# Performance work log

Hardware: AMD Instinct MI355X
Metric: run time of the kernel (lower is better)

The kernel has to match this reference:

```python
import jax, jax.numpy as jnp
import numpy as np

DIM = 1024
INTER = 1024
E = 8            # n_routed_experts
TOP_K = 2        # n_activated_experts
ROUTE_SCALE = 1.0
B, S = 2, 1024


def setup_inputs() -> dict:
    key = jax.random.key(0)
    ks = jax.random.split(key, 8)
    scale = 0.02
    x = jax.random.normal(ks[0], (B, S, DIM), dtype=jnp.float32)
    gate_w = jax.random.normal(ks[1], (DIM, E), dtype=jnp.float32) * scale
    w1 = jax.random.normal(ks[2], (E, DIM, INTER), dtype=jnp.float32) * scale
    w2 = jax.random.normal(ks[3], (E, INTER, DIM), dtype=jnp.float32) * scale
    w3 = jax.random.normal(ks[4], (E, DIM, INTER), dtype=jnp.float32) * scale
    sw1 = jax.random.normal(ks[5], (DIM, INTER), dtype=jnp.float32) * scale
    sw2 = jax.random.normal(ks[6], (INTER, DIM), dtype=jnp.float32) * scale
    sw3 = jax.random.normal(ks[7], (DIM, INTER), dtype=jnp.float32) * scale
    return {"x": x, "gate_w": gate_w, "w1": w1, "w2": w2, "w3": w3,
            "sw1": sw1, "sw2": sw2, "sw3": sw3}


def reference(x, gate_w, w1, w2, w3, sw1, sw2, sw3):
    b, s, d = x.shape
    xt = x.reshape(-1, d)                      # [T, D]
    T = xt.shape[0]

    # --- TokenChoiceTopKRouter (score_func='softmax') ---
    scores = jax.nn.softmax((xt @ gate_w).astype(jnp.float32), axis=-1)  # [T, E]
    top_scores, top_idx = jax.lax.top_k(scores, TOP_K)                   # [T, K]
    top_scores = top_scores * ROUTE_SCALE

    # Dense combine weights [T, E]: scatter top-k routing weights per token.
    cw = jnp.zeros((T, E), dtype=xt.dtype)
    cw = cw.at[jnp.arange(T)[:, None], top_idx].set(top_scores.astype(xt.dtype))

    # --- GroupedExperts: SwiGLU per routed expert ---
    h1 = jnp.einsum('td,edh->teh', xt, w1)     # [T, E, INTER]
    h3 = jnp.einsum('td,edh->teh', xt, w3)
    h = jax.nn.silu(h1) * h3
    expert_out = jnp.einsum('teh,ehd->ted', h, w2)   # [T, E, D]

    # Combine: weighted sum over activated experts (zero weight elsewhere).
    routed = jnp.einsum('ted,te->td', expert_out, cw)

    # --- Shared expert (runs on all tokens) ---
    shared = (jax.nn.silu(xt @ sw1) * (xt @ sw3)) @ sw2

    return (routed + shared).reshape(b, s, d)
```

## Files before the change

### kernel.cpp

```cpp
#include <hip/hip_runtime.h>
#include <hip/hip_bf16.h>
#include <cstdint>
#include <cstddef>

#define DIM   1024
#define INTER 1024
#define NT    2048

typedef __attribute__((ext_vector_type(4))) float  f32x4;
typedef __attribute__((ext_vector_type(8))) short  s16x8;
typedef __attribute__((ext_vector_type(8))) unsigned short u16x8;

#define WS_CNT    0u
#define WS_SLOT   256u
#define WS_ASSIGN 33024u
#define WS_WT     65792u
#define WS_WTS2   98560u
#define WS_XB     131584u
#define WS_H      4325888u
#define WS_W1T    16908800u
#define WS_W3T    33686016u
#define WS_W2T    50463232u
#define WS_SW1T   67240448u
#define WS_SW3T   69337600u
#define WS_SW2T   71434752u
#define WS_NEED   73531904u
#define WS_OBUF   WS_W1T

__device__ __forceinline__ unsigned short f2bf(float f) {
    unsigned int u = __float_as_uint(f);
    return (unsigned short)((u + 0x7fffu + ((u >> 16) & 1u)) >> 16);
}
__device__ __forceinline__ float bf2f(unsigned short v) {
    return __uint_as_float(((unsigned int)v) << 16);
}

__device__ __forceinline__ void cp16(const void* g, void* l) {
    __builtin_amdgcn_global_load_lds((const __attribute__((address_space(1))) void*)g,
                                     (__attribute__((address_space(3))) void*)l, 16, 0, 0);
}

__device__ __forceinline__ void conv_tile(const float* __restrict__ src,
                                          unsigned short* __restrict__ dst,
                                          int r0, int c0, char* smem)
{
    float (*tile)[64][65] = (float (*)[64][65])smem;
    int tid = threadIdx.x;
    int lr = tid >> 2, lcg = (tid & 3) * 16;
    #pragma unroll
    for (int h = 0; h < 2; ++h) {
        const f32x4* srow = (const f32x4*)(src + (size_t)(r0 + lr) * 1024 + c0 + h * 64 + lcg);
        #pragma unroll
        for (int q = 0; q < 4; ++q) {
            f32x4 v = srow[q];
            #pragma unroll
            for (int j = 0; j < 4; ++j) tile[h][lr][lcg + q * 4 + j] = v[j];
        }
    }
    __syncthreads();
    int dc = tid >> 2, dkg = (tid & 3) * 16;
    #pragma unroll
    for (int h = 0; h < 2; ++h) {
        u16x8 o0, o1;
        #pragma unroll
        for (int j = 0; j < 8; ++j) o0[j] = f2bf(tile[h][dkg + j][dc]);
        #pragma unroll
        for (int j = 0; j < 8; ++j) o1[j] = f2bf(tile[h][dkg + 8 + j][dc]);
        u16x8* drow = (u16x8*)(dst + (size_t)(c0 + h * 64 + dc) * 1024 + r0 + dkg);
        drow[0] = o0; drow[1] = o1;
    }
}

__global__ __launch_bounds__(256) void kfat1(
    const float* __restrict__ x, const float* __restrict__ gw,
    const float* __restrict__ w1, const float* __restrict__ w3,
    const float* __restrict__ sw1, const float* __restrict__ sw3,
    unsigned short* __restrict__ w1t, unsigned short* __restrict__ w3t,
    unsigned short* __restrict__ sw1t, unsigned short* __restrict__ sw3t,
    int* __restrict__ assign, float2* __restrict__ wts2, unsigned short* __restrict__ xb)
{
    __shared__ __align__(16) char smem[33280];
    int bid = blockIdx.x;
    if (bid < 2304) {
        int slab = bid >> 7, t = bid & 127;
        int r0 = (t >> 3) * 64, c0 = (t & 7) * 128;
        const float* src; unsigned short* dst;
        if (slab < 8)        { src = w1 + (size_t)slab * DIM * INTER;       dst = w1t + (size_t)slab * DIM * INTER; }
        else if (slab < 16)  { src = w3 + (size_t)(slab - 8) * DIM * INTER; dst = w3t + (size_t)(slab - 8) * DIM * INTER; }
        else if (slab == 16) { src = sw1; dst = sw1t; }
        else                 { src = sw3; dst = sw3t; }
        conv_tile(src, dst, r0, c0, smem);
        return;
    }
    int wid = threadIdx.x >> 6, lane = threadIdx.x & 63;
    int t = (bid - 2304) * 4 + wid;
    const float* xrow = x + (size_t)t * DIM;

    float xr[16];
    float acc[8] = {0.f,0.f,0.f,0.f,0.f,0.f,0.f,0.f};
    #pragma unroll
    for (int j = 0; j < 16; ++j) {
        float xv = xrow[j * 64 + lane];
        xr[j] = xv;
        const f32x4* g = (const f32x4*)(gw + (size_t)(j * 64 + lane) * 8);
        f32x4 g0 = g[0], g1 = g[1];
        acc[0] += xv * g0[0]; acc[1] += xv * g0[1]; acc[2] += xv * g0[2]; acc[3] += xv * g0[3];
        acc[4] += xv * g1[0]; acc[5] += xv * g1[1]; acc[6] += xv * g1[2]; acc[7] += xv * g1[3];
    }
    #pragma unroll
    for (int j = 0; j < 16; ++j) xb[(size_t)t * DIM + j * 64 + lane] = f2bf(xr[j]);

    #pragma unroll
    for (int e = 0; e < 8; ++e) {
        float v = acc[e];
        v += __shfl_xor(v, 1);  v += __shfl_xor(v, 2);  v += __shfl_xor(v, 4);
        v += __shfl_xor(v, 8);  v += __shfl_xor(v, 16); v += __shfl_xor(v, 32);
        acc[e] = v;
    }
    float mx = acc[0];
    #pragma unroll
    for (int e = 1; e < 8; ++e) mx = fmaxf(mx, acc[e]);
    float p[8]; float se = 0.f;
    #pragma unroll
    for (int e = 0; e < 8; ++e) { p[e] = expf(acc[e] - mx); se += p[e]; }
    float inv = 1.0f / se;
    int i0 = 0; float b0 = p[0];
    #pragma unroll
    for (int e = 1; e < 8; ++e) if (p[e] > b0) { b0 = p[e]; i0 = e; }
    int i1 = -1; float b1 = -1.f;
    #pragma unroll
    for (int e = 0; e < 8; ++e) if (e != i0 && p[e] > b1) { b1 = p[e]; i1 = e; }
    if (lane == 0) {
        assign[t] = i0 | (i1 << 8);
        wts2[t] = make_float2(b0 * inv, b1 * inv);
    }
}

__global__ __launch_bounds__(256) void kscatter(const int* __restrict__ assign,
                                                const float2* __restrict__ wts2,
                                                int* __restrict__ cnt,
                                                int* __restrict__ slots,
                                                float* __restrict__ wts)
{
    __shared__ int h[8], pos[8];
    int tid = threadIdx.x, lane = tid & 63;
    if (tid < 8) h[tid] = 0;
    __syncthreads();

    for (int base = 0; base < NT; base += 256) {
        int a = assign[base + tid];
        int e0 = a & 255, e1 = (a >> 8) & 255;
        #pragma unroll
        for (int e = 0; e < 8; ++e) {
            unsigned long long m0 = __ballot(e0 == e);
            unsigned long long m1 = __ballot(e1 == e);
            if (lane == 0) {
                int c = __popcll(m0) + __popcll(m1);
                if (c) atomicAdd(&h[e], c);
            }
        }
    }
    __syncthreads();
    if (tid == 0) {
        int run = 0;
        #pragma unroll
        for (int e = 0; e < 8; ++e) {
            cnt[8 + e] = run; pos[e] = run;
            cnt[e] = h[e]; run += h[e];
        }
        cnt[16] = run;
    }
    __syncthreads();

    for (int base = 0; base < NT; base += 256) {
        int t = base + tid;
        int a = assign[t];
        float2 w = wts2[t];
        int e0 = a & 255, e1 = (a >> 8) & 255;
        unsigned long long lt = (1ull << lane) - 1ull;
        #pragma unroll
        for (int e = 0; e < 8; ++e) {
            unsigned long long m0 = __ballot(e0 == e);
            unsigned long long m1 = __ballot(e1 == e);
            int c = __popcll(m0) + __popcll(m1);
            int b = 0;
            if (lane == 0 && c) b = atomicAdd(&pos[e], c);
            b = __shfl(b, 0);
            if (e0 == e) { int r = __popcll(m0 & lt);                 slots[b + r] = t * 2;     wts[b + r] = w.x; }
            if (e1 == e) { int r = __popcll(m0) + __popcll(m1 & lt);  slots[b + r] = t * 2 + 1; wts[b + r] = w.y; }
        }
    }
}

__global__ __launch_bounds__(256) void kfat2(
    const unsigned short* __restrict__ xb,
    const unsigned short* __restrict__ w1t, const unsigned short* __restrict__ w3t,
    const unsigned short* __restrict__ sw1t, const unsigned short* __restrict__ sw3t,
    const int* __restrict__ cnt, const int* __restrict__ slots,
    unsigned short* __restrict__ hbuf,
    const float* __restrict__ w2, const float* __restrict__ sw2,
    unsigned short* __restrict__ w2t, unsigned short* __restrict__ sw2t)
{
    __shared__ __align__(16) char smem[33792];
    int z = blockIdx.z;
    if (z >= 9) {
        if (blockIdx.x >= 8) return;
        int slab = z - 9;
        const float* src; unsigned short* dst;
        if (slab < 8) { src = w2 + (size_t)slab * DIM * INTER; dst = w2t + (size_t)slab * DIM * INTER; }
        else          { src = sw2; dst = sw2t; }
        conv_tile(src, dst, blockIdx.y * 64, blockIdx.x * 128, smem);
        return;
    }

    int e = z;
    int m0 = blockIdx.y * 128;
    int n0 = blockIdx.x * 64;
    int n_rows, lbase;
    if (e < 8) { n_rows = cnt[e]; lbase = cnt[8 + e]; } else { n_rows = NT; lbase = 0; }
    if (m0 >= n_rows) return;
    int rm = min(128, n_rows - m0);

    const unsigned short* b1p = (e < 8) ? (w1t + (size_t)e * DIM * INTER) : sw1t;
    const unsigned short* b3p = (e < 8) ? (w3t + (size_t)e * DIM * INTER) : sw3t;

    char* sA  = smem;
    char* sB1 = smem + 16384;
    char* sB3 = smem + 24576;
    int* rowTok  = (int*)(smem + 32768);
    int* rowSlot = (int*)(smem + 33280);

    int tid = threadIdx.x;
    if (tid < 128) {
        int r = m0 + min(tid, rm - 1);
        int slot, tok;
        if (e < 8) { slot = slots[lbase + r]; tok = slot >> 1; }
        else       { tok = r; slot = 4096 + r; }
        rowTok[tid] = tok;
        rowSlot[tid] = slot;
    }
    __syncthreads();

    int wid = tid >> 6, lane = tid & 63;
    int wr = wid >> 1, wc = wid & 1;
    int swz_st = (((lane & 7) ^ (lane >> 3)) - (lane & 7)) * 16;

    const char* pA[4];
    #pragma unroll
    for (int q = 0; q < 4; ++q) {
        int row = (q * 4 + wid) * 8 + (lane >> 3);
        pA[q] = (const char*)(xb + (size_t)rowTok[row] * DIM) + (lane & 7) * 16 + swz_st;
    }
    const char* pB1[2]; const char* pB3[2];
    #pragma unroll
    for (int q = 0; q < 2; ++q) {
        int nrow = (q * 4 + wid) * 8 + (lane >> 3);
        pB1[q] = (const char*)(b1p + (size_t)(n0 + nrow) * DIM) + (lane & 7) * 16 + swz_st;
        pB3[q] = (const char*)(b3p + (size_t)(n0 + nrow) * DIM) + (lane & 7) * 16 + swz_st;
    }

    int loA[2], loB[2];
    #pragma unroll
    for (int ks = 0; ks < 2; ++ks) {
        int ch = ((ks * 4) + (lane >> 4)) ^ (lane & 7);
        loA[ks] = (wr * 64 + (lane & 15)) * 128 + ch * 16;
        loB[ks] = (wc * 32 + (lane & 15)) * 128 + ch * 16;
    }

    f32x4 acc1[4][2], acc3[4][2];
    #pragma unroll
    for (int m = 0; m < 4; ++m)
        #pragma unroll
        for (int n = 0; n < 2; ++n) { acc1[m][n] = (f32x4){0.f,0.f,0.f,0.f}; acc3[m][n] = (f32x4){0.f,0.f,0.f,0.f}; }

    #pragma unroll
    for (int q = 0; q < 4; ++q) { cp16(pA[q], sA + (q * 4 + wid) * 1024); pA[q] += 128; }
    #pragma unroll
    for (int q = 0; q < 2; ++q) {
        cp16(pB1[q], sB1 + (q * 4 + wid) * 1024); pB1[q] += 128;
        cp16(pB3[q], sB3 + (q * 4 + wid) * 1024); pB3[q] += 128;
    }
    __syncthreads();

    for (int t = 0; t < 16; ++t) {
        #pragma unroll
        for (int ks = 0; ks < 2; ++ks) {
            s16x8 a[4];
            #pragma unroll
            for (int m = 0; m < 4; ++m)
                a[m] = *(const s16x8*)(sA + m * 2048 + loA[ks]);
            #pragma unroll
            for (int n = 0; n < 2; ++n) {
                s16x8 b1 = *(const s16x8*)(sB1 + n * 2048 + loB[ks]);
                s16x8 b3 = *(const s16x8*)(sB3 + n * 2048 + loB[ks]);
                #pragma unroll
                for (int m = 0; m < 4; ++m) {
                    acc1[m][n] = __builtin_amdgcn_mfma_f32_16x16x32_bf16(a[m], b1, acc1[m][n], 0, 0, 0);
                    acc3[m][n] = __builtin_amdgcn_mfma_f32_16x16x32_bf16(a[m], b3, acc3[m][n], 0, 0, 0);
                }
            }
        }
        __syncthreads();
        if (t < 15) {
            #pragma unroll
            for (int q = 0; q < 4; ++q) { cp16(pA[q], sA + (q * 4 + wid) * 1024); pA[q] += 128; }
            #pragma unroll
            for (int q = 0; q < 2; ++q) {
                cp16(pB1[q], sB1 + (q * 4 + wid) * 1024); pB1[q] += 128;
                cp16(pB3[q], sB3 + (q * 4 + wid) * 1024); pB3[q] += 128;
            }
            __syncthreads();
        }
    }

    #pragma unroll
    for (int m = 0; m < 4; ++m) {
        int rbase = wr * 64 + m * 16 + (lane >> 4) * 4;
        #pragma unroll
        for (int r = 0; r < 4; ++r) {
            int row = rbase + r;
            if (row < rm) {
                int hrow = rowSlot[row];
                #pragma unroll
                for (int n = 0; n < 2; ++n) {
                    float v1 = acc1[m][n][r], v3 = acc3[m][n][r];
                    float hv = (v1 / (1.0f + __expf(-v1))) * v3;
                    int col = n0 + wc * 32 + n * 16 + (lane & 15);
                    hbuf[(size_t)hrow * INTER + col] = f2bf(hv);
                }
            }
        }
    }
}

__global__ __launch_bounds__(256) void kgemm2(
    const unsigned short* __restrict__ hbuf,
    const unsigned short* __restrict__ w2t, const unsigned short* __restrict__ sw2t,
    const int* __restrict__ cnt, const int* __restrict__ slots,
    unsigned short* __restrict__ obuf)
{
    int e = blockIdx.z;
    int m0 = blockIdx.y * 128;
    int n0 = blockIdx.x * 64;
    int n_rows, lbase;
    if (e < 8) { n_rows = cnt[e]; lbase = cnt[8 + e]; } else { n_rows = NT; lbase = 0; }
    if (m0 >= n_rows) return;
    int rm = min(128, n_rows - m0);
    const unsigned short* bp = (e < 8) ? (w2t + (size_t)e * DIM * INTER) : sw2t;

    __shared__ __align__(16) short As[128 * 64];
    __shared__ __align__(16) short Bs[64 * 64];
    __shared__ int rowH[128];

    int tid = threadIdx.x;
    if (tid < 128) {
        int r = m0 + min(tid, rm - 1);
        rowH[tid] = (e < 8) ? slots[lbase + r] : (4096 + r);
    }
    __syncthreads();

    int wid = tid >> 6, lane = tid & 63;
    int wr = wid >> 1, wc = wid & 1;
    int swz_st = (((lane & 7) ^ (lane >> 3)) - (lane & 7)) * 16;

    const char* pA[4];
    #pragma unroll
    for (int q = 0; q < 4; ++q) {
        int row = (q * 4 + wid) * 8 + (lane >> 3);
        pA[q] = (const char*)(hbuf + (size_t)rowH[row] * INTER) + (lane & 7) * 16 + swz_st;
    }
    const char* pB[2];
    #pragma unroll
    for (int q = 0; q < 2; ++q) {
        int nrow = (q * 4 + wid) * 8 + (lane >> 3);
        pB[q] = (const char*)(bp + (size_t)(n0 + nrow) * INTER) + (lane & 7) * 16 + swz_st;
    }

    int loA[2], loB[2];
    #pragma unroll
    for (int ks = 0; ks < 2; ++ks) {
        int ch = ((ks * 4) + (lane >> 4)) ^ (lane & 7);
        loA[ks] = (wr * 64 + (lane & 15)) * 128 + ch * 16;
        loB[ks] = (wc * 32 + (lane & 15)) * 128 + ch * 16;
    }

    f32x4 acc[4][2];
    #pragma unroll
    for (int m = 0; m < 4; ++m)
        #pragma unroll
        for (int n = 0; n < 2; ++n) acc[m][n] = (f32x4){0.f,0.f,0.f,0.f};

    #pragma unroll
    for (int q = 0; q < 4; ++q) { cp16(pA[q], (char*)As + (q * 4 + wid) * 1024); pA[q] += 128; }
    #pragma unroll
    for (int q = 0; q < 2; ++q) { cp16(pB[q], (char*)Bs + (q * 4 + wid) * 1024); pB[q] += 128; }
    __syncthreads();

    for (int t = 0; t < 16; ++t) {
        #pragma unroll
        for (int ks = 0; ks < 2; ++ks) {
            s16x8 a[4];
            #pragma unroll
            for (int m = 0; m < 4; ++m)
                a[m] = *(const s16x8*)((const char*)As + m * 2048 + loA[ks]);
            #pragma unroll
            for (int n = 0; n < 2; ++n) {
                s16x8 b = *(const s16x8*)((const char*)Bs + n * 2048 + loB[ks]);
                #pragma unroll
                for (int m = 0; m < 4; ++m)
                    acc[m][n] = __builtin_amdgcn_mfma_f32_16x16x32_bf16(a[m], b, acc[m][n], 0, 0, 0);
            }
        }
        __syncthreads();
        if (t < 15) {
            #pragma unroll
            for (int q = 0; q < 4; ++q) { cp16(pA[q], (char*)As + (q * 4 + wid) * 1024); pA[q] += 128; }
            #pragma unroll
            for (int q = 0; q < 2; ++q) { cp16(pB[q], (char*)Bs + (q * 4 + wid) * 1024); pB[q] += 128; }
            __syncthreads();
        }
    }

    #pragma unroll
    for (int m = 0; m < 4; ++m) {
        int rbase = wr * 64 + m * 16 + (lane >> 4) * 4;
        #pragma unroll
        for (int r = 0; r < 4; ++r) {
            int row = rbase + r;
            if (row < rm) {
                int orow = rowH[row];
                #pragma unroll
                for (int n = 0; n < 2; ++n) {
                    int col = n0 + wc * 32 + n * 16 + (lane & 15);
                    obuf[(size_t)orow * DIM + col] = f2bf(acc[m][n][r]);
                }
            }
        }
    }
}

__global__ __launch_bounds__(256) void kcombine(const unsigned short* __restrict__ obuf,
                                                const float2* __restrict__ wts2,
                                                float* __restrict__ out)
{
    int gid = blockIdx.x * 256 + threadIdx.x;
    int t = gid >> 7;
    int d0 = (gid & 127) * 8;
    float2 w = wts2[t];
    u16x8 r0 = *(const u16x8*)&obuf[(size_t)(2 * t)     * DIM + d0];
    u16x8 r1 = *(const u16x8*)&obuf[(size_t)(2 * t + 1) * DIM + d0];
    u16x8 rs = *(const u16x8*)&obuf[(size_t)(4096 + t)  * DIM + d0];
    f32x4 o0, o1;
    #pragma unroll
    for (int j = 0; j < 4; ++j) o0[j] = w.x * bf2f(r0[j]) + w.y * bf2f(r1[j]) + bf2f(rs[j]);
    #pragma unroll
    for (int j = 0; j < 4; ++j) o1[j] = w.x * bf2f(r0[4+j]) + w.y * bf2f(r1[4+j]) + bf2f(rs[4+j]);
    f32x4* dst = (f32x4*)&out[(size_t)t * DIM + d0];
    dst[0] = o0; dst[1] = o1;
}

extern "C" void kernel_launch(void* const* d_in, const int* in_sizes, int n_in,
                              void* d_out, int out_size, void* d_ws, size_t ws_size,
                              hipStream_t stream) {
    const float* x      = (const float*)d_in[0];
    const float* gate_w = (const float*)d_in[1];
    const float* w1     = (const float*)d_in[2];
    const float* w2     = (const float*)d_in[3];
    const float* w3     = (const float*)d_in[4];
    const float* sw1    = (const float*)d_in[5];
    const float* sw2    = (const float*)d_in[6];
    const float* sw3    = (const float*)d_in[7];
    float* out = (float*)d_out;

    if (ws_size < (size_t)WS_NEED) return;

    char* ws = (char*)d_ws;
    int*            cnt      = (int*)(ws + WS_CNT);
    int*            slots    = (int*)(ws + WS_SLOT);
    int*            assign   = (int*)(ws + WS_ASSIGN);
    float*          wts      = (float*)(ws + WS_WT);
    float2*         wts2     = (float2*)(ws + WS_WTS2);
    unsigned short* xb       = (unsigned short*)(ws + WS_XB);
    unsigned short* hbuf     = (unsigned short*)(ws + WS_H);
    unsigned short* w1t      = (unsigned short*)(ws + WS_W1T);
    unsigned short* w3t      = (unsigned short*)(ws + WS_W3T);
    unsigned short* w2t      = (unsigned short*)(ws + WS_W2T);
    unsigned short* sw1t     = (unsigned short*)(ws + WS_SW1T);
    unsigned short* sw3t     = (unsigned short*)(ws + WS_SW3T);
    unsigned short* sw2t     = (unsigned short*)(ws + WS_SW2T);
    unsigned short* obuf     = (unsigned short*)(ws + WS_OBUF);

    kfat1<<<dim3(2816), 256, 0, stream>>>(x, gate_w, w1, w3, sw1, sw3,
                                          w1t, w3t, sw1t, sw3t, assign, wts2, xb);
    kscatter<<<dim3(1), 256, 0, stream>>>(assign, wts2, cnt, slots, wts);
    kfat2<<<dim3(16, 16, 18), 256, 0, stream>>>(xb, w1t, w3t, sw1t, sw3t, cnt, slots, hbuf,
                                                w2, sw2, w2t, sw2t);
    kgemm2<<<dim3(16, 16, 9), 256, 0, stream>>>(hbuf, w2t, sw2t, cnt, slots, obuf);
    kcombine<<<dim3(1024), 256, 0, stream>>>(obuf, wts2, out);
}
```

Baseline: 129.9 us.

## Load GEMM A operand directly to registers with double-buffering; rework transpose tile

Both grouped GEMM kernels now skip staging the gathered A rows through LDS and instead load each lane's MFMA A fragments straight from global memory into registers. These loads are double-buffered one K-step ahead to hide latency and cut LDS traffic and footprint, which may raise occupancy. Each wave now loads its own A rows, so A reads are duplicated across the two column waves and register pressure rises from the doubled fragment arrays. The fp32-to-bf16 transpose tile is also rewritten with a padded 132-stride LDS layout and a different thread mapping, giving wider coalesced loads and single 16-byte stores.

```diff
diff --git a/kernel.cpp b/kernel.cpp
--- a/kernel.cpp
+++ b/kernel.cpp
@@ -44,30 +44,31 @@
                                           unsigned short* __restrict__ dst,
                                           int r0, int c0, char* smem)
 {
-    float (*tile)[64][65] = (float (*)[64][65])smem;
+    float* ldsf = (float*)smem;
     int tid = threadIdx.x;
-    int lr = tid >> 2, lcg = (tid & 3) * 16;
-    #pragma unroll
-    for (int h = 0; h < 2; ++h) {
-        const f32x4* srow = (const f32x4*)(src + (size_t)(r0 + lr) * 1024 + c0 + h * 64 + lcg);
-        #pragma unroll
-        for (int q = 0; q < 4; ++q) {
-            f32x4 v = srow[q];
-            #pragma unroll
-            for (int j = 0; j < 4; ++j) tile[h][lr][lcg + q * 4 + j] = v[j];
-        }
-    }
-    __syncthreads();
-    int dc = tid >> 2, dkg = (tid & 3) * 16;
-    #pragma unroll
-    for (int h = 0; h < 2; ++h) {
-        u16x8 o0, o1;
-        #pragma unroll
-        for (int j = 0; j < 8; ++j) o0[j] = f2bf(tile[h][dkg + j][dc]);
-        #pragma unroll
-        for (int j = 0; j < 8; ++j) o1[j] = f2bf(tile[h][dkg + 8 + j][dc]);
-        u16x8* drow = (u16x8*)(dst + (size_t)(c0 + h * 64 + dc) * 1024 + r0 + dkg);
-        drow[0] = o0; drow[1] = o1;
+    {
+        int row  = tid >> 5;
+        int colw = (tid & 31) * 4;
+        const float* s = src + (size_t)(r0 + row) * 1024 + c0 + colw;
+        float* d = ldsf + row * 132 + colw;
+        #pragma unroll
+        for (int i = 0; i < 8; ++i) {
+            f32x4 v = *(const f32x4*)(s + (size_t)i * 8 * 1024);
+            *(f32x4*)(d + i * 8 * 132) = v;
+        }
+    }
+    __syncthreads();
+    {
+        int rr    = (tid & 7) * 8;
+        int cbase = tid >> 3;
+        #pragma unroll
+        for (int i = 0; i < 4; ++i) {
+            int c = i * 32 + cbase;
+            u16x8 o;
+            #pragma unroll
+            for (int j = 0; j < 8; ++j) o[j] = f2bf(ldsf[(rr + j) * 132 + c]);
+            *(u16x8*)(dst + (size_t)(c0 + c) * 1024 + r0 + rr) = o;
+        }
     }
 }
 
@@ -79,7 +80,7 @@
     unsigned short* __restrict__ sw1t, unsigned short* __restrict__ sw3t,
     int* __restrict__ assign, float2* __restrict__ wts2, unsigned short* __restrict__ xb)
 {
-    __shared__ __align__(16) char smem[33280];
+    __shared__ __align__(16) char smem[33792];
     int bid = blockIdx.x;
     if (bid < 2304) {
         int slab = bid >> 7, t = bid & 127;
@@ -224,11 +225,10 @@
     const unsigned short* b1p = (e < 8) ? (w1t + (size_t)e * DIM * INTER) : sw1t;
     const unsigned short* b3p = (e < 8) ? (w3t + (size_t)e * DIM * INTER) : sw3t;
 
-    char* sA  = smem;
-    char* sB1 = smem + 16384;
-    char* sB3 = smem + 24576;
-    int* rowTok  = (int*)(smem + 32768);
-    int* rowSlot = (int*)(smem + 33280);
+    char* sB1 = smem;
+    char* sB3 = smem + 8192;
+    int* rowTok  = (int*)(smem + 16384);
+    int* rowSlot = (int*)(smem + 16896);
 
     int tid = threadIdx.x;
     if (tid < 128) {
@@ -245,11 +245,11 @@
     int wr = wid >> 1, wc = wid & 1;
     int swz_st = (((lane & 7) ^ (lane >> 3)) - (lane & 7)) * 16;
 
-    const char* pA[4];
-    #pragma unroll
-    for (int q = 0; q < 4; ++q) {
-        int row = (q * 4 + wid) * 8 + (lane >> 3);
-        pA[q] = (const char*)(xb + (size_t)rowTok[row] * DIM) + (lane & 7) * 16 + swz_st;
+    const unsigned short* pAr[4];
+    #pragma unroll
+    for (int m = 0; m < 4; ++m) {
+        int row = wr * 64 + m * 16 + (lane & 15);
+        pAr[m] = xb + (size_t)rowTok[row] * DIM + (lane >> 4) * 8;
     }
     const char* pB1[2]; const char* pB3[2];
     #pragma unroll
@@ -259,11 +259,10 @@
         pB3[q] = (const char*)(b3p + (size_t)(n0 + nrow) * DIM) + (lane & 7) * 16 + swz_st;
     }
 
-    int loA[2], loB[2];
+    int loB[2];
     #pragma unroll
     for (int ks = 0; ks < 2; ++ks) {
         int ch = ((ks * 4) + (lane >> 4)) ^ (lane & 7);
-        loA[ks] = (wr * 64 + (lane & 15)) * 128 + ch * 16;
         loB[ks] = (wc * 32 + (lane & 15)) * 128 + ch * 16;
     }
 
@@ -273,37 +272,44 @@
         #pragma unroll
         for (int n = 0; n < 2; ++n) { acc1[m][n] = (f32x4){0.f,0.f,0.f,0.f}; acc3[m][n] = (f32x4){0.f,0.f,0.f,0.f}; }
 
-    #pragma unroll
-    for (int q = 0; q < 4; ++q) { cp16(pA[q], sA + (q * 4 + wid) * 1024); pA[q] += 128; }
     #pragma unroll
     for (int q = 0; q < 2; ++q) {
         cp16(pB1[q], sB1 + (q * 4 + wid) * 1024); pB1[q] += 128;
         cp16(pB3[q], sB3 + (q * 4 + wid) * 1024); pB3[q] += 128;
     }
-    __syncthreads();
-
+    s16x8 a[2][4][2];
+    #pragma unroll
+    for (int m = 0; m < 4; ++m)
+        #pragma unroll
+        for (int ks = 0; ks < 2; ++ks)
+            a[0][m][ks] = *(const s16x8*)(pAr[m] + ks * 32);
+    __syncthreads();
+
+    #pragma unroll
     for (int t = 0; t < 16; ++t) {
+        const int cur = t & 1;
+        if (t < 15) {
+            #pragma unroll
+            for (int m = 0; m < 4; ++m)
+                #pragma unroll
+                for (int ks = 0; ks < 2; ++ks)
+                    a[cur ^ 1][m][ks] = *(const s16x8*)(pAr[m] + (t + 1) * 64 + ks * 32);
+        }
         #pragma unroll
         for (int ks = 0; ks < 2; ++ks) {
-            s16x8 a[4];
-            #pragma unroll
-            for (int m = 0; m < 4; ++m)
-                a[m] = *(const s16x8*)(sA + m * 2048 + loA[ks]);
             #pragma unroll
             for (int n = 0; n < 2; ++n) {
                 s16x8 b1 = *(const s16x8*)(sB1 + n * 2048 + loB[ks]);
                 s16x8 b3 = *(const s16x8*)(sB3 + n * 2048 + loB[ks]);
                 #pragma unroll
                 for (int m = 0; m < 4; ++m) {
-                    acc1[m][n] = __builtin_amdgcn_mfma_f32_16x16x32_bf16(a[m], b1, acc1[m][n], 0, 0, 0);
-                    acc3[m][n] = __builtin_amdgcn_mfma_f32_16x16x32_bf16(a[m], b3, acc3[m][n], 0, 0, 0);
+                    acc1[m][n] = __builtin_amdgcn_mfma_f32_16x16x32_bf16(a[cur][m][ks], b1, acc1[m][n], 0, 0, 0);
+                    acc3[m][n] = __builtin_amdgcn_mfma_f32_16x16x32_bf16(a[cur][m][ks], b3, acc3[m][n], 0, 0, 0);
                 }
             }
         }
         __syncthreads();
         if (t < 15) {
-            #pragma unroll
-            for (int q = 0; q < 4; ++q) { cp16(pA[q], sA + (q * 4 + wid) * 1024); pA[q] += 128; }
             #pragma unroll
             for (int q = 0; q < 2; ++q) {
                 cp16(pB1[q], sB1 + (q * 4 + wid) * 1024); pB1[q] += 128;
@@ -348,7 +354,6 @@
     int rm = min(128, n_rows - m0);
     const unsigned short* bp = (e < 8) ? (w2t + (size_t)e * DIM * INTER) : sw2t;
 
-    __shared__ __align__(16) short As[128 * 64];
     __shared__ __align__(16) short Bs[64 * 64];
     __shared__ int rowH[128];
 
@@ -363,11 +368,11 @@
     int wr = wid >> 1, wc = wid & 1;
     int swz_st = (((lane & 7) ^ (lane >> 3)) - (lane & 7)) * 16;
 
-    const char* pA[4];
-    #pragma unroll
-    for (int q = 0; q < 4; ++q) {
-        int row = (q * 4 + wid) * 8 + (lane >> 3);
-        pA[q] = (const char*)(hbuf + (size_t)rowH[row] * INTER) + (lane & 7) * 16 + swz_st;
+    const unsigned short* pAr[4];
+    #pragma unroll
+    for (int m = 0; m < 4; ++m) {
+        int row = wr * 64 + m * 16 + (lane & 15);
+        pAr[m] = hbuf + (size_t)rowH[row] * INTER + (lane >> 4) * 8;
     }
     const char* pB[2];
     #pragma unroll
@@ -376,11 +381,10 @@
         pB[q] = (const char*)(bp + (size_t)(n0 + nrow) * INTER) + (lane & 7) * 16 + swz_st;
     }
 
-    int loA[2], loB[2];
+    int loB[2];
     #pragma unroll
     for (int ks = 0; ks < 2; ++ks) {
         int ch = ((ks * 4) + (lane >> 4)) ^ (lane & 7);
-        loA[ks] = (wr * 64 + (lane & 15)) * 128 + ch * 16;
         loB[ks] = (wc * 32 + (lane & 15)) * 128 + ch * 16;
     }
 
@@ -391,30 +395,37 @@
         for (int n = 0; n < 2; ++n) acc[m][n] = (f32x4){0.f,0.f,0.f,0.f};
 
     #pragma unroll
-    for (int q = 0; q < 4; ++q) { cp16(pA[q], (char*)As + (q * 4 + wid) * 1024); pA[q] += 128; }
-    #pragma unroll
     for (int q = 0; q < 2; ++q) { cp16(pB[q], (char*)Bs + (q * 4 + wid) * 1024); pB[q] += 128; }
-    __syncthreads();
-
+    s16x8 a[2][4][2];
+    #pragma unroll
+    for (int m = 0; m < 4; ++m)
+        #pragma unroll
+        for (int ks = 0; ks < 2; ++ks)
+            a[0][m][ks] = *(const s16x8*)(pAr[m] + ks * 32);
+    __syncthreads();
+
+    #pragma unroll
     for (int t = 0; t < 16; ++t) {
+        const int cur = t & 1;
+        if (t < 15) {
+            #pragma unroll
+            for (int m = 0; m < 4; ++m)
+                #pragma unroll
+                for (int ks = 0; ks < 2; ++ks)
+                    a[cur ^ 1][m][ks] = *(const s16x8*)(pAr[m] + (t + 1) * 64 + ks * 32);
+        }
         #pragma unroll
         for (int ks = 0; ks < 2; ++ks) {
-            s16x8 a[4];
-            #pragma unroll
-            for (int m = 0; m < 4; ++m)
-                a[m] = *(const s16x8*)((const char*)As + m * 2048 + loA[ks]);
             #pragma unroll
             for (int n = 0; n < 2; ++n) {
                 s16x8 b = *(const s16x8*)((const char*)Bs + n * 2048 + loB[ks]);
                 #pragma unroll
                 for (int m = 0; m < 4; ++m)
-                    acc[m][n] = __builtin_amdgcn_mfma_f32_16x16x32_bf16(a[m], b, acc[m][n], 0, 0, 0);
+                    acc[m][n] = __builtin_amdgcn_mfma_f32_16x16x32_bf16(a[cur][m][ks], b, acc[m][n], 0, 0, 0);
             }
         }
         __syncthreads();
         if (t < 15) {
-            #pragma unroll
-            for (int q = 0; q < 4; ++q) { cp16(pA[q], (char*)As + (q * 4 + wid) * 1024); pA[q] += 128; }
             #pragma unroll
             for (int q = 0; q < 2; ++q) { cp16(pB[q], (char*)Bs + (q * 4 + wid) * 1024); pB[q] += 128; }
             __syncthreads();
```

Measured after the change: 202.2 us. 55.7% more time.
